# Kernel optimization log

Hardware: AMD Instinct MI355X
Metric: run time of the kernel (lower is better)

The kernel has to match this reference:

```python
import jax, jax.numpy as jnp
import numpy as np

N_NODES = 10000
N_EDGES = 80000
IN_DIM = 1024
HID = 4096
OUT = 256


def sage_conv(x, src, dst, W_l, b_l, W_r, num_nodes):
    # mean aggregation of source-node features onto target nodes
    msg = x[src]                                            # [E, D] gather
    agg = jax.ops.segment_sum(msg, dst, num_segments=num_nodes)   # [N, D]
    cnt = jax.ops.segment_sum(jnp.ones((src.shape[0],), x.dtype), dst,
                              num_segments=num_nodes)       # [N]
    mean = agg / jnp.clip(cnt, 1.0)[:, None]                # isolated nodes -> 0
    # lin_l(mean) + lin_r(x); lin_r has no bias in PyG SAGEConv
    return mean @ W_l.T + b_l + x @ W_r.T


def setup_inputs() -> dict:
    key = jax.random.key(0)
    ks = jax.random.split(key, 6)
    x = jax.random.normal(ks[0], (N_NODES, IN_DIM), dtype=jnp.float32)
    edge_index = jax.random.randint(ks[1], (2, N_EDGES), 0, N_NODES, dtype=jnp.int32)
    s1 = 1.0 / np.sqrt(IN_DIM)
    s2 = 1.0 / np.sqrt(HID)
    W1_l = jax.random.normal(ks[2], (HID, IN_DIM), dtype=jnp.float32) * s1
    b1_l = jnp.zeros((HID,), jnp.float32)
    W1_r = jax.random.normal(ks[3], (HID, IN_DIM), dtype=jnp.float32) * s1
    W2_l = jax.random.normal(ks[4], (OUT, HID), dtype=jnp.float32) * s2
    b2_l = jnp.zeros((OUT,), jnp.float32)
    W2_r = jax.random.normal(ks[5], (OUT, HID), dtype=jnp.float32) * s2
    return {"x": x, "edge_index": edge_index, "W1_l": W1_l, "b1_l": b1_l,
            "W1_r": W1_r, "W2_l": W2_l, "b2_l": b2_l, "W2_r": W2_r}


def reference(x, edge_index, W1_l, b1_l, W1_r, W2_l, b2_l, W2_r):
    src, dst = edge_index[0], edge_index[1]
    h = sage_conv(x, src, dst, W1_l, b1_l, W1_r, N_NODES)   # [N, 4096]
    h = jax.nn.relu(h)
    # dropout is identity in eval mode
    out = sage_conv(h, src, dst, W2_l, b2_l, W2_r, N_NODES)  # [N, 256]
    return jax.nn.log_softmax(out, axis=1)
```

## Files before the change

### kernel.cpp

```cpp
#include <hip/hip_runtime.h>
#include <cstdint>
#include <cstddef>

#define DEVINL __device__ __forceinline__

typedef __bf16 bf16x8 __attribute__((ext_vector_type(8)));
typedef float f32x4 __attribute__((ext_vector_type(4)));

static constexpr int NN = 10000;
static constexpr int NE = 80000;
static constexpr int IN_DIM = 1024;
static constexpr int HID = 4096;
static constexpr int OUTD = 256;
static constexpr int M_PAD = 10112;

DEVINL unsigned short f2bf(float f) {
  unsigned int u = __builtin_bit_cast(unsigned int, f);
  u += 0x7fffu + ((u >> 16) & 1u);
  return (unsigned short)(u >> 16);
}
DEVINL float bf2f(unsigned short h) {
  unsigned int u = ((unsigned int)h) << 16;
  return __builtin_bit_cast(float, u);
}

DEVINL void ld_lds16(const void* g, void* l) {
  __builtin_amdgcn_global_load_lds(
      (const __attribute__((address_space(1))) unsigned int*)g,
      (__attribute__((address_space(3))) unsigned int*)l, 16, 0, 0);
}

static constexpr int PREP_B1 = 8192;
static constexpr int PREP_B2 = PREP_B1 + 2048;
static constexpr int PREP_B3 = PREP_B2 + 10000;
static constexpr int PREP_NB = PREP_B3 + 313;

__global__ __launch_bounds__(256) void prep_kernel(
    const float* __restrict__ W1l, const float* __restrict__ W1r,
    const float* __restrict__ W2l, const float* __restrict__ W2r,
    const float* __restrict__ x, const int* __restrict__ dst,
    unsigned short* __restrict__ w1cat, unsigned short* __restrict__ w2cat,
    unsigned short* __restrict__ x_bf, int* __restrict__ deg) {
  int b = blockIdx.x;
  int t = threadIdx.x;
  if (b < PREP_B1) {
    int g = b * 256 + t;
    int n = g >> 9;
    int kg = g & 511;
    const float* s = (kg < 256) ? (W1l + (size_t)n * 1024 + kg * 4)
                                : (W1r + (size_t)n * 1024 + (kg - 256) * 4);
    float4 v = *(const float4*)s;
    ushort4 p = {f2bf(v.x), f2bf(v.y), f2bf(v.z), f2bf(v.w)};
    ((ushort4*)w1cat)[g] = p;
  } else if (b < PREP_B2) {
    int g = (b - PREP_B1) * 256 + t;
    int n = g >> 10;
    int kg = g & 1023;
    const float* s = (n < 256) ? (W2l + (size_t)n * 4096 + kg * 4)
                               : (W2r + (size_t)(n - 256) * 4096 + kg * 4);
    float4 v = *(const float4*)s;
    ushort4 p = {f2bf(v.x), f2bf(v.y), f2bf(v.z), f2bf(v.w)};
    ((ushort4*)w2cat)[g] = p;
  } else if (b < PREP_B3) {
    int g = (b - PREP_B2) * 256 + t;
    int i = g >> 8;
    int kg = g & 255;
    float4 v = ((const float4*)(x + (size_t)i * IN_DIM))[kg];
    ushort4 p = {f2bf(v.x), f2bf(v.y), f2bf(v.z), f2bf(v.w)};
    ((ushort4*)(x_bf + (size_t)i * IN_DIM))[kg] = p;
  } else {
    int e = (b - PREP_B3) * 256 + t;
    if (e < NE) atomicAdd(&deg[dst[e]], 1);
  }
}

__global__ __launch_bounds__(1024) void scan_kernel(const int* __restrict__ deg,
                                                    int* __restrict__ offs,
                                                    int* __restrict__ cur) {
  __shared__ int part[1024];
  constexpr int NPT = 10;
  int t = threadIdx.x;
  int base = t * NPT;
  int s = 0;
  for (int j = 0; j < NPT; ++j) {
    int n = base + j;
    s += (n < NN) ? deg[n] : 0;
  }
  part[t] = s;
  __syncthreads();
  for (int o = 1; o < 1024; o <<= 1) {
    int v = (t >= o) ? part[t - o] : 0;
    __syncthreads();
    part[t] += v;
    __syncthreads();
  }
  int pre = (t > 0) ? part[t - 1] : 0;
  for (int j = 0; j < NPT; ++j) {
    int n = base + j;
    if (n < NN) {
      offs[n] = pre;
      cur[n] = pre;
      pre += deg[n];
    }
  }
  if (t == 1023) offs[NN] = part[1023];
}

__global__ void bin_kernel(const int* __restrict__ src, const int* __restrict__ dst,
                           int* __restrict__ cur, int* __restrict__ csr) {
  int e = blockIdx.x * 256 + threadIdx.x;
  if (e < NE) {
    int p = atomicAdd(&cur[dst[e]], 1);
    csr[p] = src[e];
  }
}

__global__ __launch_bounds__(256) void gather1_kernel(unsigned short* __restrict__ x_bf,
                                                      const int* __restrict__ offs,
                                                      const int* __restrict__ csr,
                                                      unsigned short* __restrict__ A1) {
  int i = blockIdx.x;
  int t = threadIdx.x;
  unsigned short* row = A1 + (size_t)i * 1024;
  if (i >= NN) {
    ushort4 z = {0, 0, 0, 0};
    ((ushort4*)row)[t] = z;
    ((ushort4*)(x_bf + (size_t)i * 1024))[t] = z;
    return;
  }
  int beg = offs[i], end = offs[i + 1];
  float4 a0 = {0.f, 0.f, 0.f, 0.f}, a1 = {0.f, 0.f, 0.f, 0.f};
  int j = beg;
  for (; j + 2 <= end; j += 2) {
    int s0 = __builtin_amdgcn_readfirstlane(csr[j]);
    int s1 = __builtin_amdgcn_readfirstlane(csr[j + 1]);
    ushort4 u0 = ((const ushort4*)(x_bf + (size_t)s0 * IN_DIM))[t];
    ushort4 u1 = ((const ushort4*)(x_bf + (size_t)s1 * IN_DIM))[t];
    a0.x += bf2f(u0.x); a0.y += bf2f(u0.y); a0.z += bf2f(u0.z); a0.w += bf2f(u0.w);
    a1.x += bf2f(u1.x); a1.y += bf2f(u1.y); a1.z += bf2f(u1.z); a1.w += bf2f(u1.w);
  }
  if (j < end) {
    int s0 = __builtin_amdgcn_readfirstlane(csr[j]);
    ushort4 u0 = ((const ushort4*)(x_bf + (size_t)s0 * IN_DIM))[t];
    a0.x += bf2f(u0.x); a0.y += bf2f(u0.y); a0.z += bf2f(u0.z); a0.w += bf2f(u0.w);
  }
  float inv = 1.0f / (float)max(end - beg, 1);
  ushort4 pa = {f2bf((a0.x + a1.x) * inv), f2bf((a0.y + a1.y) * inv),
                f2bf((a0.z + a1.z) * inv), f2bf((a0.w + a1.w) * inv)};
  ((ushort4*)row)[t] = pa;
}

__global__ __launch_bounds__(512) void gemm1_8ph_kernel(
    const unsigned short* __restrict__ A,
    const unsigned short* __restrict__ A2,
    const unsigned short* __restrict__ Bt,
    const float* __restrict__ bias,
    unsigned short* __restrict__ C) {
  constexpr int BM = 256, BN = 256, BK = 64;
  constexpr int K = 2048, N = 4096;
  constexpr int NT = K / BK;
  constexpr int NUMM = 40, NUMN = 16, GM = 8, NPG = GM * NUMN;

  __shared__ unsigned short Asm[2][BM * BK];
  __shared__ unsigned short Bsm[2][BN * BK];

  const int pid = blockIdx.x;
  const int gid = pid / NPG;
  const int first_m = gid * GM;
  const int local = pid % NPG;
  const int pm = first_m + (local % GM);
  const int pn = local / GM;
  const long tm0 = (long)pm * BM;
  const long tn0 = (long)pn * BN;

  const int tid = threadIdx.x;
  const int lane = tid & 63;
  const int wave = tid >> 6;
  const int quad = lane >> 4;
  const int l16 = lane & 15;
  const int l7 = l16 & 7;
  const int wr = wave >> 2;
  const int wc = wave & 3;
  const int wm = wr * 128;
  const int wn = wc * 64;

  f32x4 acc[8][4];
#pragma unroll
  for (int i = 0; i < 8; ++i)
#pragma unroll
    for (int j = 0; j < 4; ++j) acc[i][j] = (f32x4){0.f, 0.f, 0.f, 0.f};

  size_t aOffE[4], bOffE[4];
#pragma unroll
  for (int s = 0; s < 4; ++s) {
    int c = s * 512 + tid;
    int r = c >> 3;
    int g = (c & 7) ^ (r & 7);
    long ra = tm0 + r;
    if (ra > M_PAD - 1) ra = M_PAD - 1;
    aOffE[s] = (size_t)ra * 1024 + g * 8;
    bOffE[s] = (size_t)(tn0 + r) * K + g * 8;
  }

#define STAGE_A(kt, buf)                                                        \
  {                                                                             \
    const unsigned short* ab_ = ((kt) < NT / 2) ? A : A2;                       \
    const int ka_ = ((kt) & (NT / 2 - 1)) * BK;                                 \
    _Pragma("unroll") for (int s_ = 0; s_ < 4; ++s_)                            \
        ld_lds16(ab_ + aOffE[s_] + ka_, &Asm[(buf)][(s_ * 512 + wave * 64) * 8]); \
  }
#define STAGE_B(kt, buf)                                                        \
  {                                                                             \
    const int k0_ = (kt)*BK;                                                    \
    _Pragma("unroll") for (int s_ = 0; s_ < 4; ++s_)                            \
        ld_lds16(Bt + bOffE[s_] + k0_, &Bsm[(buf)][(s_ * 512 + wave * 64) * 8]); \
  }

  STAGE_A(0, 0)
  STAGE_B(0, 0)

  for (int kt = 0; kt < NT; ++kt) {
    const int buf = kt & 1;
    if (kt + 1 < NT) {
      STAGE_A(kt + 1, buf ^ 1)
      STAGE_B(kt + 1, buf ^ 1)
      asm volatile("s_waitcnt vmcnt(8)" ::: "memory");
    } else {
      asm volatile("s_waitcnt vmcnt(0)" ::: "memory");
    }
    __builtin_amdgcn_s_barrier();

    const unsigned short* As = Asm[buf];
    const unsigned short* Bs = Bsm[buf];

    bf16x8 bv[2][4];
#pragma unroll
    for (int kk = 0; kk < 2; ++kk)
#pragma unroll
      for (int nj = 0; nj < 4; ++nj) {
        int rb = wn + nj * 16 + l16;
        int p = (kk * 4 + quad) ^ l7;
        bv[kk][nj] = *(const bf16x8*)(Bs + rb * BK + p * 8);
      }

#pragma unroll
    for (int q = 0; q < 4; ++q) {
      bf16x8 af[2][2];
#pragma unroll
      for (int kk = 0; kk < 2; ++kk)
#pragma unroll
        for (int i = 0; i < 2; ++i) {
          int ra = wm + (q * 2 + i) * 16 + l16;
          int p = (kk * 4 + quad) ^ l7;
          af[kk][i] = *(const bf16x8*)(As + ra * BK + p * 8);
        }
      __builtin_amdgcn_s_barrier();
      asm volatile("s_waitcnt lgkmcnt(0)" ::: "memory");
      __builtin_amdgcn_s_setprio(1);
#pragma unroll
      for (int kk = 0; kk < 2; ++kk)
#pragma unroll
        for (int i = 0; i < 2; ++i)
#pragma unroll
          for (int nj = 0; nj < 4; ++nj)
            acc[q * 2 + i][nj] = __builtin_amdgcn_mfma_f32_16x16x32_bf16(
                af[kk][i], bv[kk][nj], acc[q * 2 + i][nj], 0, 0, 0);
      __builtin_amdgcn_s_setprio(0);
      __builtin_amdgcn_s_barrier();
    }
  }
#undef STAGE_A
#undef STAGE_B

#pragma unroll
  for (int mi = 0; mi < 8; ++mi) {
    long m0 = tm0 + wm + mi * 16 + quad * 4;
#pragma unroll
    for (int nj = 0; nj < 4; ++nj) {
      int n = (int)tn0 + wn + nj * 16 + l16;
      float bvs = bias[n];
#pragma unroll
      for (int r = 0; r < 4; ++r) {
        long m = m0 + r;
        if (m < M_PAD) {
          float v = fmaxf(acc[mi][nj][r] + bvs, 0.0f);
          C[(size_t)m * N + n] = f2bf(v);
        }
      }
    }
  }
}

template <int BM, int BN, int BK, int K, int KSPLIT, int N, int NUMM, int NUMN, int GM,
          int EPI, int NWY, bool ASPLIT>
__global__ __launch_bounds__(256) void gemm_kernel(const unsigned short* __restrict__ A,
                                                   const unsigned short* __restrict__ A2,
                                                   const unsigned short* __restrict__ Bt,
                                                   const float* __restrict__ bias,
                                                   void* __restrict__ C0out) {
  constexpr int MGR = 4 / NWY;
  constexpr int MI = BM / 16 / MGR;
  constexpr int NI = 4;
  constexpr int CPR = BK / 8;
  constexpr int SA = BM * CPR / 256;
  constexpr int SB = BN * CPR / 256;
  constexpr int KK = BK / 32;
  constexpr int KS = K / KSPLIT;
  constexpr int AS = ASPLIT ? K / 2 : K;
  __shared__ unsigned short Asm[BM * BK];
  __shared__ unsigned short Bsm[BN * BK];

  constexpr int NPG = GM * NUMN;
  const int pid = blockIdx.x;
  const int gid = pid / NPG;
  const int first_m = gid * GM;
  const int sz = (NUMM - first_m < GM) ? (NUMM - first_m) : GM;
  const int local = pid % NPG;
  const int pm = first_m + local % sz;
  const int pn = local / sz;
  const int koff = (KSPLIT > 1) ? (int)blockIdx.y * KS : 0;

  const int tid = threadIdx.x;
  const int lane = tid & 63;
  const int wave = tid >> 6;
  const int quad = lane >> 4;
  const int l16 = lane & 15;
  const int wm = (wave % MGR) * (BM / MGR);
  const int wn = (wave / MGR) * 64;
  const long tm0 = (long)pm * BM;
  const long tn0 = (long)pn * BN;

  f32x4 acc[MI][NI];
#pragma unroll
  for (int i = 0; i < MI; ++i)
#pragma unroll
    for (int j = 0; j < NI; ++j) acc[i][j] = (f32x4){0.f, 0.f, 0.f, 0.f};

  size_t aOff[SA];
  unsigned short* aDst[SA];
  const unsigned short* bSrc[SB];
  unsigned short* bDst[SB];
#pragma unroll
  for (int s = 0; s < SA; ++s) {
    int c = s * 256 + wave * 64 + lane;
    int r = c / CPR;
    int g = (c % CPR) ^ (r & 7);
    aOff[s] = (size_t)(tm0 + r) * AS + koff + g * 8;
    aDst[s] = Asm + s * 2048 + wave * 512;
  }
#pragma unroll
  for (int s = 0; s < SB; ++s) {
    int c = s * 256 + wave * 64 + lane;
    int r = c / CPR;
    int g = (c % CPR) ^ (r & 7);
    bSrc[s] = Bt + (size_t)(tn0 + r) * K + koff + g * 8;
    bDst[s] = Bsm + s * 2048 + wave * 512;
  }

  const int l7 = l16 & 7;

  for (int k0 = 0; k0 < KS; k0 += BK) {
    const unsigned short* ab = (!ASPLIT || k0 < K / 2) ? A : A2;
    const int ka = ASPLIT ? (k0 & (K / 2 - 1)) : k0;
#pragma unroll
    for (int s = 0; s < SA; ++s) ld_lds16(ab + aOff[s] + ka, aDst[s]);
#pragma unroll
    for (int s = 0; s < SB; ++s) ld_lds16(bSrc[s] + k0, bDst[s]);
    __syncthreads();

#pragma unroll
    for (int kk = 0; kk < KK; ++kk) {
      const int p = (kk * 4 + quad) ^ l7;
      bf16x8 af[MI], bv[NI];
#pragma unroll
      for (int i = 0; i < MI; ++i) {
        int ra = wm + i * 16 + l16;
        af[i] = *(const bf16x8*)(Asm + ra * BK + p * 8);
      }
#pragma unroll
      for (int j = 0; j < NI; ++j) {
        int rb = wn + j * 16 + l16;
        bv[j] = *(const bf16x8*)(Bsm + rb * BK + p * 8);
      }
#pragma unroll
      for (int i = 0; i < MI; ++i)
#pragma unroll
        for (int j = 0; j < NI; ++j)
          acc[i][j] = __builtin_amdgcn_mfma_f32_16x16x32_bf16(af[i], bv[j], acc[i][j], 0, 0, 0);
    }
    __syncthreads();
  }

  if (EPI == 1) {
    unsigned short* C = (unsigned short*)C0out;
#pragma unroll
    for (int i = 0; i < MI; ++i) {
      long m0 = tm0 + wm + i * 16 + quad * 4;
#pragma unroll
      for (int j = 0; j < NI; ++j) {
        int n = (int)tn0 + wn + j * 16 + l16;
        float bvs = bias[n];
#pragma unroll
        for (int r = 0; r < 4; ++r) {
          float v = acc[i][j][r] + bvs;
          v = fmaxf(v, 0.0f);
          C[(size_t)(m0 + r) * N + n] = f2bf(v);
        }
      }
    }
  } else {
    unsigned short* C = (unsigned short*)C0out + (size_t)blockIdx.y * NUMM * BM * N;
#pragma unroll
    for (int i = 0; i < MI; ++i) {
      long m0 = tm0 + wm + i * 16 + quad * 4;
#pragma unroll
      for (int j = 0; j < NI; ++j) {
        int n = (int)tn0 + wn + j * 16 + l16;
#pragma unroll
        for (int r = 0; r < 4; ++r) C[(size_t)(m0 + r) * N + n] = f2bf(acc[i][j][r]);
      }
    }
  }
}

__global__ __launch_bounds__(128) void gather2_final_kernel(const unsigned short* __restrict__ P,
                                                            const int* __restrict__ offs,
                                                            const int* __restrict__ csr,
                                                            const float* __restrict__ b2,
                                                            float* __restrict__ out) {
  int i = blockIdx.x;
  int t = threadIdx.x;
  const unsigned short* P1 = P + (size_t)M_PAD * 512;
  int beg = offs[i], end = offs[i + 1];
  float a0 = 0.f, a1 = 0.f, c0 = 0.f, c1 = 0.f;
  int j = beg;
  for (; j + 2 <= end; j += 2) {
    int s0 = __builtin_amdgcn_readfirstlane(csr[j]);
    int s1 = __builtin_amdgcn_readfirstlane(csr[j + 1]);
    unsigned int u0 = ((const unsigned int*)(P + (size_t)s0 * 512))[t];
    unsigned int w0 = ((const unsigned int*)(P1 + (size_t)s0 * 512))[t];
    unsigned int u1 = ((const unsigned int*)(P + (size_t)s1 * 512))[t];
    unsigned int w1 = ((const unsigned int*)(P1 + (size_t)s1 * 512))[t];
    a0 += bf2f((unsigned short)(u0 & 0xffffu)) + bf2f((unsigned short)(w0 & 0xffffu));
    a1 += bf2f((unsigned short)(u0 >> 16)) + bf2f((unsigned short)(w0 >> 16));
    c0 += bf2f((unsigned short)(u1 & 0xffffu)) + bf2f((unsigned short)(w1 & 0xffffu));
    c1 += bf2f((unsigned short)(u1 >> 16)) + bf2f((unsigned short)(w1 >> 16));
  }
  if (j < end) {
    int s0 = __builtin_amdgcn_readfirstlane(csr[j]);
    unsigned int u0 = ((const unsigned int*)(P + (size_t)s0 * 512))[t];
    unsigned int w0 = ((const unsigned int*)(P1 + (size_t)s0 * 512))[t];
    a0 += bf2f((unsigned short)(u0 & 0xffffu)) + bf2f((unsigned short)(w0 & 0xffffu));
    a1 += bf2f((unsigned short)(u0 >> 16)) + bf2f((unsigned short)(w0 >> 16));
  }
  float inv = 1.0f / (float)max(end - beg, 1);
  float2 bv = ((const float2*)b2)[t];
  unsigned int su = ((const unsigned int*)(P + (size_t)i * 512))[128 + t];
  unsigned int sw = ((const unsigned int*)(P1 + (size_t)i * 512))[128 + t];
  float pv0 = bf2f((unsigned short)(su & 0xffffu)) + bf2f((unsigned short)(sw & 0xffffu));
  float pv1 = bf2f((unsigned short)(su >> 16)) + bf2f((unsigned short)(sw >> 16));
  float v0 = (a0 + c0) * inv + bv.x + pv0;
  float v1 = (a1 + c1) * inv + bv.y + pv1;

  __shared__ float sm[2], ss[2];
  int w = t >> 6;
  float m = fmaxf(v0, v1);
#pragma unroll
  for (int o = 32; o > 0; o >>= 1) m = fmaxf(m, __shfl_xor(m, o, 64));
  if ((t & 63) == 0) sm[w] = m;
  __syncthreads();
  m = fmaxf(sm[0], sm[1]);

  float s = __expf(v0 - m) + __expf(v1 - m);
#pragma unroll
  for (int o = 32; o > 0; o >>= 1) s += __shfl_xor(s, o, 64);
  if ((t & 63) == 0) ss[w] = s;
  __syncthreads();
  float ls = logf(ss[0] + ss[1]);

  float2 o2 = {v0 - m - ls, v1 - m - ls};
  ((float2*)(out + (size_t)i * OUTD))[t] = o2;
}

static constexpr size_t OFF_A1 = 0;
static constexpr size_t OFF_XBF = OFF_A1 + (size_t)M_PAD * 1024 * 2;
static constexpr size_t OFF_W1 = OFF_XBF + (size_t)M_PAD * 1024 * 2;
static constexpr size_t OFF_HB = OFF_W1 + (size_t)HID * 2048 * 2;
static constexpr size_t OFF_W2 = OFF_HB + (size_t)M_PAD * HID * 2;
static constexpr size_t OFF_DEG = OFF_W2 + (size_t)512 * HID * 2;
static constexpr size_t OFF_OFFS = OFF_DEG + (size_t)NN * 4;
static constexpr size_t OFF_CUR = OFF_OFFS + (size_t)(NN + 4) * 4;
static constexpr size_t OFF_CSR = OFF_CUR + (size_t)NN * 4;
static constexpr size_t OFF_P = OFF_A1;

extern "C" void kernel_launch(void* const* d_in, const int* in_sizes, int n_in,
                              void* d_out, int out_size, void* d_ws, size_t ws_size,
                              hipStream_t stream) {
  const float* x = (const float*)d_in[0];
  const int* ei = (const int*)d_in[1];
  const int* src = ei;
  const int* dst = ei + NE;
  const float* W1_l = (const float*)d_in[2];
  const float* b1_l = (const float*)d_in[3];
  const float* W1_r = (const float*)d_in[4];
  const float* W2_l = (const float*)d_in[5];
  const float* b2_l = (const float*)d_in[6];
  const float* W2_r = (const float*)d_in[7];
  float* out = (float*)d_out;

  char* ws = (char*)d_ws;
  unsigned short* A1 = (unsigned short*)(ws + OFF_A1);
  unsigned short* x_bf = (unsigned short*)(ws + OFF_XBF);
  unsigned short* w1cat = (unsigned short*)(ws + OFF_W1);
  unsigned short* h_b = (unsigned short*)(ws + OFF_HB);
  unsigned short* w2cat = (unsigned short*)(ws + OFF_W2);
  int* deg = (int*)(ws + OFF_DEG);
  int* offs = (int*)(ws + OFF_OFFS);
  int* cur = (int*)(ws + OFF_CUR);
  int* csr = (int*)(ws + OFF_CSR);
  unsigned short* P = (unsigned short*)(ws + OFF_P);

  hipMemsetAsync(deg, 0, (size_t)NN * 4, stream);

  prep_kernel<<<PREP_NB, 256, 0, stream>>>(W1_l, W1_r, W2_l, W2_r, x, dst,
                                           w1cat, w2cat, x_bf, deg);
  scan_kernel<<<1, 1024, 0, stream>>>(deg, offs, cur);
  bin_kernel<<<(NE + 255) / 256, 256, 0, stream>>>(src, dst, cur, csr);

  gather1_kernel<<<M_PAD, 256, 0, stream>>>(x_bf, offs, csr, A1);

  gemm1_8ph_kernel<<<40 * 16, 512, 0, stream>>>(A1, x_bf, w1cat, b1_l, h_b);

  gemm_kernel<64, 256, 64, 4096, 2, 512, 158, 2, 1, 3, 4, false>
      <<<dim3(158 * 2, 2), 256, 0, stream>>>(h_b, nullptr, w2cat, nullptr, P);

  gather2_final_kernel<<<NN, 128, 0, stream>>>(P, offs, csr, b2_l, out);
}
```

Measured before the change: 477.6 us.

## Interleave next-tile global-to-LDS prefetch into MFMA phases of GEMM1 main loop

The GEMM1 loop no longer issues all A and B prefetches for the next K tile up front followed by a vmcnt wait. It now issues the A prefetch during the first MFMA phase and the B prefetch during the second, and waits for vmcnt(0) only at the end of the last phase. Sched barriers pin the instruction order. The aim is to spread memory issue across the compute phases and hide load latency behind MFMA work. In exchange, ordering gets more fragile: the LDS buffer being written must not still be in use, and the lgkmcnt counts have to stay correct.

New measurement: 461.3 us. -3.4%, faster.

```diff
diff --git a/kernel.cpp b/kernel.cpp
--- a/kernel.cpp
+++ b/kernel.cpp
@@ -159,7 +159,7 @@
   constexpr int BM = 256, BN = 256, BK = 64;
   constexpr int K = 2048, N = 4096;
   constexpr int NT = K / BK;
-  constexpr int NUMM = 40, NUMN = 16, GM = 8, NPG = GM * NUMN;
+  constexpr int NUMN = 16, GM = 8, NPG = GM * NUMN;
 
   __shared__ unsigned short Asm[2][BM * BK];
   __shared__ unsigned short Bsm[2][BN * BK];
@@ -179,10 +179,8 @@
   const int quad = lane >> 4;
   const int l16 = lane & 15;
   const int l7 = l16 & 7;
-  const int wr = wave >> 2;
-  const int wc = wave & 3;
-  const int wm = wr * 128;
-  const int wn = wc * 64;
+  const int wm = (wave >> 2) * 128;
+  const int wn = (wave & 3) * 64;
 
   f32x4 acc[8][4];
 #pragma unroll
@@ -202,34 +200,27 @@
     bOffE[s] = (size_t)(tn0 + r) * K + g * 8;
   }
 
-#define STAGE_A(kt, buf)                                                        \
-  {                                                                             \
-    const unsigned short* ab_ = ((kt) < NT / 2) ? A : A2;                       \
-    const int ka_ = ((kt) & (NT / 2 - 1)) * BK;                                 \
-    _Pragma("unroll") for (int s_ = 0; s_ < 4; ++s_)                            \
+#define STAGE_A(kt, buf)                                                          \
+  {                                                                               \
+    const unsigned short* ab_ = ((kt) < NT / 2) ? A : A2;                         \
+    const int ka_ = ((kt) & (NT / 2 - 1)) * BK;                                   \
+    _Pragma("unroll") for (int s_ = 0; s_ < 4; ++s_)                              \
         ld_lds16(ab_ + aOffE[s_] + ka_, &Asm[(buf)][(s_ * 512 + wave * 64) * 8]); \
   }
-#define STAGE_B(kt, buf)                                                        \
-  {                                                                             \
-    const int k0_ = (kt)*BK;                                                    \
-    _Pragma("unroll") for (int s_ = 0; s_ < 4; ++s_)                            \
+#define STAGE_B(kt, buf)                                                          \
+  {                                                                               \
+    const int k0_ = (kt)*BK;                                                      \
+    _Pragma("unroll") for (int s_ = 0; s_ < 4; ++s_)                              \
         ld_lds16(Bt + bOffE[s_] + k0_, &Bsm[(buf)][(s_ * 512 + wave * 64) * 8]); \
   }
 
   STAGE_A(0, 0)
   STAGE_B(0, 0)
+  asm volatile("s_waitcnt vmcnt(0)" ::: "memory");
+  __builtin_amdgcn_s_barrier();
 
   for (int kt = 0; kt < NT; ++kt) {
     const int buf = kt & 1;
-    if (kt + 1 < NT) {
-      STAGE_A(kt + 1, buf ^ 1)
-      STAGE_B(kt + 1, buf ^ 1)
-      asm volatile("s_waitcnt vmcnt(8)" ::: "memory");
-    } else {
-      asm volatile("s_waitcnt vmcnt(0)" ::: "memory");
-    }
-    __builtin_amdgcn_s_barrier();
-
     const unsigned short* As = Asm[buf];
     const unsigned short* Bs = Bsm[buf];
 
@@ -237,25 +228,49 @@
 #pragma unroll
     for (int kk = 0; kk < 2; ++kk)
 #pragma unroll
-      for (int nj = 0; nj < 4; ++nj) {
-        int rb = wn + nj * 16 + l16;
-        int p = (kk * 4 + quad) ^ l7;
-        bv[kk][nj] = *(const bf16x8*)(Bs + rb * BK + p * 8);
-      }
-
-#pragma unroll
-    for (int q = 0; q < 4; ++q) {
+      for (int nj = 0; nj < 4; ++nj)
+        bv[kk][nj] =
+            *(const bf16x8*)(Bs + (wn + nj * 16 + l16) * BK + (((kk * 4 + quad) ^ l7) * 8));
+    {
       bf16x8 af[2][2];
 #pragma unroll
       for (int kk = 0; kk < 2; ++kk)
 #pragma unroll
-        for (int i = 0; i < 2; ++i) {
-          int ra = wm + (q * 2 + i) * 16 + l16;
-          int p = (kk * 4 + quad) ^ l7;
-          af[kk][i] = *(const bf16x8*)(As + ra * BK + p * 8);
-        }
+        for (int i = 0; i < 2; ++i)
+          af[kk][i] =
+              *(const bf16x8*)(As + (wm + i * 16 + l16) * BK + (((kk * 4 + quad) ^ l7) * 8));
+      if (kt + 1 < NT) STAGE_A(kt + 1, buf ^ 1)
+      asm volatile("s_waitcnt lgkmcnt(8)" ::: "memory");
       __builtin_amdgcn_s_barrier();
       asm volatile("s_waitcnt lgkmcnt(0)" ::: "memory");
+      __builtin_amdgcn_sched_barrier(0);
+      __builtin_amdgcn_s_setprio(1);
+#pragma unroll
+      for (int kk = 0; kk < 2; ++kk)
+#pragma unroll
+        for (int i = 0; i < 2; ++i)
+#pragma unroll
+          for (int nj = 0; nj < 4; ++nj)
+            acc[i][nj] = __builtin_amdgcn_mfma_f32_16x16x32_bf16(af[kk][i], bv[kk][nj],
+                                                                 acc[i][nj], 0, 0, 0);
+      __builtin_amdgcn_s_setprio(0);
+      __builtin_amdgcn_s_barrier();
+      __builtin_amdgcn_sched_barrier(0);
+    }
+
+#pragma unroll
+    for (int q = 1; q < 4; ++q) {
+      bf16x8 af[2][2];
+#pragma unroll
+      for (int kk = 0; kk < 2; ++kk)
+#pragma unroll
+        for (int i = 0; i < 2; ++i)
+          af[kk][i] = *(const bf16x8*)(As + (wm + (q * 2 + i) * 16 + l16) * BK +
+                                       (((kk * 4 + quad) ^ l7) * 8));
+      if (q == 1 && kt + 1 < NT) STAGE_B(kt + 1, buf ^ 1)
+      __builtin_amdgcn_s_barrier();
+      asm volatile("s_waitcnt lgkmcnt(0)" ::: "memory");
+      __builtin_amdgcn_sched_barrier(0);
       __builtin_amdgcn_s_setprio(1);
 #pragma unroll
       for (int kk = 0; kk < 2; ++kk)
@@ -266,7 +281,11 @@
             acc[q * 2 + i][nj] = __builtin_amdgcn_mfma_f32_16x16x32_bf16(
                 af[kk][i], bv[kk][nj], acc[q * 2 + i][nj], 0, 0, 0);
       __builtin_amdgcn_s_setprio(0);
+      if (q == 3) {
+        asm volatile("s_waitcnt vmcnt(0)" ::: "memory");
+      }
       __builtin_amdgcn_s_barrier();
+      __builtin_amdgcn_sched_barrier(0);
     }
   }
 #undef STAGE_A
```
